# Optimization experiments

Hardware: AMD Instinct MI355X
Metric: run time of the kernel (lower is better)

Reference implementation:

```python
import jax, jax.numpy as jnp
import numpy as np
from jax import lax

L = 2048      # sentence length
V = 50000     # vocab size
E = 512       # embedding dim
HD = 512      # per-direction hidden (hidden_dim // 2)
H = 1024      # hidden_dim
T = 48        # tagset size
START, STOP = 46, 47
NEG = -10000.0


def setup_inputs() -> dict:
    key = jax.random.key(0)
    ks = iter(jax.random.split(key, 40))
    def n(shape, s=0.1):
        return jax.random.normal(next(ks), shape, dtype=jnp.float32) * s
    inp = {"sentence": jax.random.randint(next(ks), (L,), 0, V, dtype=jnp.int32)}
    inp["embedding"] = n((V, E), 1.0)
    for l, din in ((0, E), (1, H)):
        for d in ("", "r"):
            inp[f"w_ih_l{l}{d}"] = n((4 * HD, din))
            inp[f"w_hh_l{l}{d}"] = n((4 * HD, HD))
            inp[f"b_ih_l{l}{d}"] = n((4 * HD,))
            inp[f"b_hh_l{l}{d}"] = n((4 * HD,))
    inp["h0"] = n((4, HD), 1.0)
    inp["c0"] = n((4, HD), 1.0)
    inp["W_tag"] = n((T, H))
    inp["b_tag"] = n((T,))
    tr = n((T, T), 1.0)
    inp["transitions"] = tr.at[START, :].set(NEG).at[:, STOP].set(NEG)
    return inp


def _lstm_dir(x, w_ih, w_hh, b_ih, b_hh, h, c, reverse):
    # PyTorch LSTM cell, gates ordered (i, f, g, o). x: [L, Din]
    pre = x @ w_ih.T + (b_ih + b_hh)  # [L, 4*HD]
    def step(carry, p):
        h, c = carry
        g = p + h @ w_hh.T
        i, f, gg, o = jnp.split(g, 4)
        i, f, o = jax.nn.sigmoid(i), jax.nn.sigmoid(f), jax.nn.sigmoid(o)
        c = f * c + i * jnp.tanh(gg)
        h = o * jnp.tanh(c)
        return (h, c), h
    _, hs = lax.scan(step, (h, c), pre, reverse=reverse)
    return hs  # [L, HD], time-aligned with input


def _viterbi(feats, transitions):
    # max-plus recurrence over the tagset, vectorized per timestep
    init = jnp.full((T,), NEG, dtype=feats.dtype).at[START].set(0.0)
    def step(fv, feat):
        scores = fv[None, :] + transitions  # [next_tag, prev_tag]
        bp = jnp.argmax(scores, axis=1)
        return jnp.max(scores, axis=1) + feat, bp
    fv, bps = lax.scan(step, init, feats)  # bps: [L, T]
    terminal = fv + transitions[STOP]
    best = jnp.argmax(terminal)
    score = terminal[best]
    def back(tag, bp):
        prev = bp[tag]
        return prev, prev
    _, ys = lax.scan(back, best, bps, reverse=True)
    # ys[0] == START (dropped); path is tags for t = 0..L-1
    path = jnp.concatenate([ys[1:], best[None]])
    return score, path


def reference(sentence, embedding,
              w_ih_l0, w_hh_l0, b_ih_l0, b_hh_l0,
              w_ih_l0r, w_hh_l0r, b_ih_l0r, b_hh_l0r,
              w_ih_l1, w_hh_l1, b_ih_l1, b_hh_l1,
              w_ih_l1r, w_hh_l1r, b_ih_l1r, b_hh_l1r,
              h0, c0, W_tag, b_tag, transitions):
    embeds = embedding[sentence]  # [L, E]
    l0 = jnp.concatenate([
        _lstm_dir(embeds, w_ih_l0, w_hh_l0, b_ih_l0, b_hh_l0, h0[0], c0[0], False),
        _lstm_dir(embeds, w_ih_l0r, w_hh_l0r, b_ih_l0r, b_hh_l0r, h0[1], c0[1], True),
    ], axis=-1)  # [L, H]
    l1 = jnp.concatenate([
        _lstm_dir(l0, w_ih_l1, w_hh_l1, b_ih_l1, b_hh_l1, h0[2], c0[2], False),
        _lstm_dir(l0, w_ih_l1r, w_hh_l1r, b_ih_l1r, b_hh_l1r, h0[3], c0[3], True),
    ], axis=-1)  # [L, H]
    feats = l1 @ W_tag.T + b_tag  # [L, T]
    score, path = _viterbi(feats, transitions)
    return score, path
```

## Files before the change

kernel.cpp:

```cpp
#include <hip/hip_runtime.h>
#include <hip/hip_bf16.h>

#define L_SEQ 2048
#define HDIM 512
#define NGATE4 2048
#define TAGS 48
#define START_TAG 46
#define STOP_TAG 47
#define NWG 16

#define BM 64
#define BN 64
#define BK 32
#define LDT 68

__global__ __launch_bounds__(256, 2)
void gemm_abt(const float* __restrict__ A, const float* __restrict__ B,
              const float* __restrict__ bias1, const float* __restrict__ bias2,
              float* __restrict__ C, int M, int N, int K,
              const int* __restrict__ gather)
{
  __shared__ float As[BK][LDT];
  __shared__ float Bs[BK][LDT];
  const int tid = threadIdx.x;
  const int m0 = blockIdx.x * BM;
  const int n0 = blockIdx.y * BN;
  const int tm = tid >> 4, tn = tid & 15;
  const int lr = tid >> 2, lk = (tid & 3) * 8;

  float acc[4][4];
#pragma unroll
  for (int i = 0; i < 4; ++i)
#pragma unroll
    for (int c = 0; c < 4; ++c) acc[i][c] = 0.f;

  const int am = m0 + lr;
  const float* arow = gather ? (A + (size_t)gather[am] * (size_t)K)
                             : (A + (size_t)am * (size_t)K);
  const int bn = n0 + lr;
  const float* brow = B + (size_t)bn * (size_t)K;
  const bool bok = (bn < N);

  for (int kt = 0; kt < K; kt += BK) {
    const float4 a0 = *(const float4*)(arow + kt + lk);
    const float4 a1 = *(const float4*)(arow + kt + lk + 4);
    float4 b0 = make_float4(0.f, 0.f, 0.f, 0.f);
    float4 b1 = make_float4(0.f, 0.f, 0.f, 0.f);
    if (bok) {
      b0 = *(const float4*)(brow + kt + lk);
      b1 = *(const float4*)(brow + kt + lk + 4);
    }
    As[lk + 0][lr] = a0.x; As[lk + 1][lr] = a0.y; As[lk + 2][lr] = a0.z; As[lk + 3][lr] = a0.w;
    As[lk + 4][lr] = a1.x; As[lk + 5][lr] = a1.y; As[lk + 6][lr] = a1.z; As[lk + 7][lr] = a1.w;
    Bs[lk + 0][lr] = b0.x; Bs[lk + 1][lr] = b0.y; Bs[lk + 2][lr] = b0.z; Bs[lk + 3][lr] = b0.w;
    Bs[lk + 4][lr] = b1.x; Bs[lk + 5][lr] = b1.y; Bs[lk + 6][lr] = b1.z; Bs[lk + 7][lr] = b1.w;
    __syncthreads();
#pragma unroll
    for (int kk = 0; kk < BK; ++kk) {
      const float4 av = *(const float4*)&As[kk][tm * 4];
      const float4 bv = *(const float4*)&Bs[kk][tn * 4];
      const float aa[4] = {av.x, av.y, av.z, av.w};
      const float bb[4] = {bv.x, bv.y, bv.z, bv.w};
#pragma unroll
      for (int i = 0; i < 4; ++i)
#pragma unroll
        for (int c = 0; c < 4; ++c)
          acc[i][c] += aa[i] * bb[c];
    }
    __syncthreads();
  }

  float bsum[4];
#pragma unroll
  for (int c = 0; c < 4; ++c) {
    const int n = n0 + tn * 4 + c;
    float bb = 0.f;
    if (n < N) { bb = bias1[n]; if (bias2) bb += bias2[n]; }
    bsum[c] = bb;
  }
#pragma unroll
  for (int i = 0; i < 4; ++i) {
    const int m = m0 + tm * 4 + i;
#pragma unroll
    for (int c = 0; c < 4; ++c) {
      const int n = n0 + tn * 4 + c;
      if (n < N) C[(size_t)m * N + n] = acc[i][c] + bsum[c];
    }
  }
}

__global__ __launch_bounds__(512, 1)
void lstm_layer(const float* __restrict__ pre_f, const float* __restrict__ pre_r,
                const float* __restrict__ whh_f, const float* __restrict__ whh_r,
                const float* __restrict__ h0, const float* __restrict__ c0,
                int hcrow_base,
                float* __restrict__ hs_out,
                int* __restrict__ slots)
{
  const int dir = blockIdx.x & 1;
  const int wg  = blockIdx.x >> 1;
  const float* pre = dir ? pre_r : pre_f;
  const float* whh = dir ? whh_r : whh_f;
  int* myslots = slots + dir * NWG;
  const int tid = threadIdx.x;
  const int lane = tid & 63;
  const int wave = tid >> 6;
  const int q = lane & 15;
  const int jj = (wave << 2) | (lane >> 4);
  const int j = wg * 32 + jj;
  const bool leader = (q == 0);
  const int hc = (hcrow_base + dir) * HDIM;

  __shared__ float h_lds[HDIM];

  float w[4][8][4];
#pragma unroll
  for (int g = 0; g < 4; ++g) {
    const float* wr = whh + (size_t)(g * HDIM + j) * HDIM;
#pragma unroll
    for (int i = 0; i < 8; ++i) {
      const int kb = 32 * q + 4 * ((i + q) & 7);
      const float4 v = *(const float4*)(wr + kb);
      w[g][i][0] = v.x; w[g][i][1] = v.y; w[g][i][2] = v.z; w[g][i][3] = v.w;
    }
  }
  h_lds[tid] = h0[hc + tid];
  float cst = leader ? c0[hc + j] : 0.f;
  __syncthreads();

  float p[4], pn[4];
  {
    const int t0 = dir ? (L_SEQ - 1) : 0;
#pragma unroll
    for (int g = 0; g < 4; ++g)
      p[g] = leader ? pre[(size_t)t0 * NGATE4 + g * HDIM + j] : 0.f;
  }

  for (int s = 0; s < L_SEQ; ++s) {
    const int t = dir ? (L_SEQ - 1 - s) : s;
#pragma unroll
    for (int g = 0; g < 4; ++g) pn[g] = 0.f;
    if (leader && (s + 1 < L_SEQ)) {
      const int tnx = dir ? (L_SEQ - 2 - s) : (s + 1);
#pragma unroll
      for (int g = 0; g < 4; ++g)
        pn[g] = pre[(size_t)tnx * NGATE4 + g * HDIM + j];
    }

    float a[4] = {0.f, 0.f, 0.f, 0.f};
#pragma unroll
    for (int i = 0; i < 8; ++i) {
      const int kb = 32 * q + 4 * ((i + q) & 7);
      const float4 hv = *(const float4*)&h_lds[kb];
      const float hh[4] = {hv.x, hv.y, hv.z, hv.w};
#pragma unroll
      for (int g = 0; g < 4; ++g)
#pragma unroll
        for (int c = 0; c < 4; ++c)
          a[g] += w[g][i][c] * hh[c];
    }
#pragma unroll
    for (int m = 1; m < 16; m <<= 1)
#pragma unroll
      for (int g = 0; g < 4; ++g)
        a[g] += __shfl_xor(a[g], m, 64);

    if (leader) {
      const float gi = p[0] + a[0];
      const float gf = p[1] + a[1];
      const float gg = p[2] + a[2];
      const float go = p[3] + a[3];
      const float si = 1.f / (1.f + __expf(-gi));
      const float sf = 1.f / (1.f + __expf(-gf));
      const float tg = 1.f - 2.f / (__expf(2.f * gg) + 1.f);
      const float so = 1.f / (1.f + __expf(-go));
      cst = sf * cst + si * tg;
      const float th = 1.f - 2.f / (__expf(2.f * cst) + 1.f);
      const float h = so * th;
      __hip_atomic_store(&hs_out[(size_t)t * 1024 + dir * HDIM + j], h,
                         __ATOMIC_RELAXED, __HIP_MEMORY_SCOPE_AGENT);
    }
#pragma unroll
    for (int g = 0; g < 4; ++g) p[g] = pn[g];

    if (s == L_SEQ - 1) break;

    __syncthreads();
    if (tid == 0)
      __hip_atomic_store(&myslots[wg], s + 1, __ATOMIC_RELEASE,
                         __HIP_MEMORY_SCOPE_AGENT);
    if (wave == 0) {
      for (;;) {
        const int v = (lane < NWG)
            ? __hip_atomic_load(&myslots[lane], __ATOMIC_ACQUIRE,
                                __HIP_MEMORY_SCOPE_AGENT)
            : 0x7fffffff;
        if (__all(v > s)) break;
      }
    }
    __syncthreads();
    {
      const size_t base = (size_t)t * 1024 + dir * HDIM;
      h_lds[tid] = __hip_atomic_load(&hs_out[base + tid], __ATOMIC_RELAXED,
                                     __HIP_MEMORY_SCOPE_AGENT);
    }
    __syncthreads();
  }
}

__global__ __launch_bounds__(192, 1)
void viterbi_kernel(const float* __restrict__ feats,
                    const float* __restrict__ trans,
                    int* __restrict__ bp,
                    float* __restrict__ out)
{
  __shared__ float fv[TAGS];
  __shared__ float fvn[TAGS];
  const int tid = threadIdx.x;
  const int lane = tid & 63;
  const int wave = tid >> 6;
  const int q = lane & 3;
  const int j = wave * 16 + (lane >> 2);

  float trr[12];
#pragma unroll
  for (int kk = 0; kk < 12; ++kk) trr[kk] = trans[j * TAGS + q * 12 + kk];

  if (tid < TAGS) fv[tid] = (tid == START_TAG) ? 0.f : -10000.f;
  __syncthreads();

  for (int t = 0; t < L_SEQ; ++t) {
    const float ft = feats[t * TAGS + j];
    float best = -3.0e38f;
    int bi = 0;
#pragma unroll
    for (int kk = 0; kk < 12; ++kk) {
      const int k = q * 12 + kk;
      const float sc = fv[k] + trr[kk];
      if (sc > best) { best = sc; bi = k; }
    }
#pragma unroll
    for (int m = 1; m < 4; m <<= 1) {
      const float ov = __shfl_xor(best, m, 64);
      const int oi = __shfl_xor(bi, m, 64);
      if (ov > best || (ov == best && oi < bi)) { best = ov; bi = oi; }
    }
    __syncthreads();
    if (q == 0) {
      bp[t * TAGS + j] = bi;
      fv[j] = best + ft;
    }
    __syncthreads();
  }

  if (tid < TAGS) fvn[tid] = fv[tid] + trans[STOP_TAG * TAGS + tid];
  __syncthreads();
  if (tid == 0) {
    float best = -3.0e38f;
    int bi = 0;
    for (int k = 0; k < TAGS; ++k) {
      const float v = fvn[k];
      if (v > best) { best = v; bi = k; }
    }
    out[0] = best;
    int cur = bi;
    out[1 + (L_SEQ - 1)] = (float)cur;
    for (int t = L_SEQ - 2; t >= 0; --t) {
      cur = bp[(t + 1) * TAGS + cur];
      out[1 + t] = (float)cur;
    }
  }
}

extern "C" void kernel_launch(void* const* d_in, const int* in_sizes, int n_in,
                              void* d_out, int out_size, void* d_ws, size_t ws_size,
                              hipStream_t stream)
{
  const int*   sentence  = (const int*)  d_in[0];
  const float* embedding = (const float*)d_in[1];
  const float* w_ih_l0   = (const float*)d_in[2];
  const float* w_hh_l0   = (const float*)d_in[3];
  const float* b_ih_l0   = (const float*)d_in[4];
  const float* b_hh_l0   = (const float*)d_in[5];
  const float* w_ih_l0r  = (const float*)d_in[6];
  const float* w_hh_l0r  = (const float*)d_in[7];
  const float* b_ih_l0r  = (const float*)d_in[8];
  const float* b_hh_l0r  = (const float*)d_in[9];
  const float* w_ih_l1   = (const float*)d_in[10];
  const float* w_hh_l1   = (const float*)d_in[11];
  const float* b_ih_l1   = (const float*)d_in[12];
  const float* b_hh_l1   = (const float*)d_in[13];
  const float* w_ih_l1r  = (const float*)d_in[14];
  const float* w_hh_l1r  = (const float*)d_in[15];
  const float* b_ih_l1r  = (const float*)d_in[16];
  const float* b_hh_l1r  = (const float*)d_in[17];
  const float* h0        = (const float*)d_in[18];
  const float* c0        = (const float*)d_in[19];
  const float* W_tag     = (const float*)d_in[20];
  const float* b_tag     = (const float*)d_in[21];
  const float* trans     = (const float*)d_in[22];

  float* ws    = (float*)d_ws;
  float* pre_f = ws;
  float* pre_r = pre_f + (size_t)L_SEQ * NGATE4;
  float* l0out = pre_r + (size_t)L_SEQ * NGATE4;
  float* l1out = l0out + (size_t)L_SEQ * 1024;
  float* feats = l1out + (size_t)L_SEQ * 1024;
  int*   slots = (int*)(feats + (size_t)L_SEQ * TAGS);
  int*   bp    = slots + 4 * NWG;

  (void)hipMemsetAsync(slots, 0, 4 * NWG * sizeof(int), stream);

  dim3 blk(256);
  dim3 gfull(L_SEQ / BM, NGATE4 / BN);
  gemm_abt<<<gfull, blk, 0, stream>>>(embedding, w_ih_l0, b_ih_l0, b_hh_l0,
                                      pre_f, L_SEQ, NGATE4, 512, sentence);
  gemm_abt<<<gfull, blk, 0, stream>>>(embedding, w_ih_l0r, b_ih_l0r, b_hh_l0r,
                                      pre_r, L_SEQ, NGATE4, 512, sentence);
  lstm_layer<<<2 * NWG, 512, 0, stream>>>(pre_f, pre_r, w_hh_l0, w_hh_l0r,
                                          h0, c0, 0, l0out, slots);
  gemm_abt<<<gfull, blk, 0, stream>>>(l0out, w_ih_l1, b_ih_l1, b_hh_l1,
                                      pre_f, L_SEQ, NGATE4, 1024, nullptr);
  gemm_abt<<<gfull, blk, 0, stream>>>(l0out, w_ih_l1r, b_ih_l1r, b_hh_l1r,
                                      pre_r, L_SEQ, NGATE4, 1024, nullptr);
  lstm_layer<<<2 * NWG, 512, 0, stream>>>(pre_f, pre_r, w_hh_l1, w_hh_l1r,
                                          h0, c0, 2, l1out, slots + 2 * NWG);
  dim3 gfeat(L_SEQ / BM, 1);
  gemm_abt<<<gfeat, blk, 0, stream>>>(l1out, W_tag, b_tag, nullptr,
                                      feats, L_SEQ, TAGS, 1024, nullptr);
  viterbi_kernel<<<1, 192, 0, stream>>>(feats, trans, bp, (float*)d_out);
}
```

Before: 16.04 ms.

## Spread LSTM workgroups across XCDs and vectorize recurrent matvec accumulators

The recurrent LSTM kernel now launches 128 workgroups and keeps only those with blockIdx%8 in {0,1}. Round-robin dispatch should then place all 32 active workgroups on the same one or two XCDs, so the per-step cross-workgroup flag sync and h exchange stay within a shared L2 rather than crossing dies. The weight registers and matvec accumulation are also rewritten as float4 variables with per-lane float4 accumulators, reduced at the end, to aid register allocation and packed FMA. The extra idle workgroups add launch overhead, and the XCD placement depends on dispatch order, which the hardware does not guarantee.

```diff
diff --git a/kernel.cpp b/kernel.cpp
--- a/kernel.cpp
+++ b/kernel.cpp
@@ -8,6 +8,8 @@
 #define START_TAG 46
 #define STOP_TAG 47
 #define NWG 16
+
+typedef float4 f4;
 
 #define BM 64
 #define BN 64
@@ -89,6 +91,22 @@
   }
 }
 
+#define LOADW(g) { const float* wr = whh + (size_t)((g) * HDIM + j) * HDIM + 32 * q; \
+  w##g##0 = *(const f4*)(wr + 4 * ((0 + q) & 7)); \
+  w##g##1 = *(const f4*)(wr + 4 * ((1 + q) & 7)); \
+  w##g##2 = *(const f4*)(wr + 4 * ((2 + q) & 7)); \
+  w##g##3 = *(const f4*)(wr + 4 * ((3 + q) & 7)); \
+  w##g##4 = *(const f4*)(wr + 4 * ((4 + q) & 7)); \
+  w##g##5 = *(const f4*)(wr + 4 * ((5 + q) & 7)); \
+  w##g##6 = *(const f4*)(wr + 4 * ((6 + q) & 7)); \
+  w##g##7 = *(const f4*)(wr + 4 * ((7 + q) & 7)); }
+
+#define FMA4(A_, W_, H_) { A_.x += (W_).x * (H_).x; A_.y += (W_).y * (H_).y; \
+                           A_.z += (W_).z * (H_).z; A_.w += (W_).w * (H_).w; }
+
+#define FI(i) { const f4 hv_ = *(const f4*)&h_lds[32 * q + 4 * (((i) + q) & 7)]; \
+  FMA4(acc0, w0##i, hv_) FMA4(acc1, w1##i, hv_) FMA4(acc2, w2##i, hv_) FMA4(acc3, w3##i, hv_) }
+
 __global__ __launch_bounds__(512, 1)
 void lstm_layer(const float* __restrict__ pre_f, const float* __restrict__ pre_r,
                 const float* __restrict__ whh_f, const float* __restrict__ whh_r,
@@ -97,8 +115,10 @@
                 float* __restrict__ hs_out,
                 int* __restrict__ slots)
 {
-  const int dir = blockIdx.x & 1;
-  const int wg  = blockIdx.x >> 1;
+  const int sel = blockIdx.x & 7;
+  if (sel > 1) return;
+  const int dir = sel;
+  const int wg  = blockIdx.x >> 3;
   const float* pre = dir ? pre_r : pre_f;
   const float* whh = dir ? whh_r : whh_f;
   int* myslots = slots + dir * NWG;
@@ -113,63 +133,58 @@
 
   __shared__ float h_lds[HDIM];
 
-  float w[4][8][4];
-#pragma unroll
-  for (int g = 0; g < 4; ++g) {
-    const float* wr = whh + (size_t)(g * HDIM + j) * HDIM;
-#pragma unroll
-    for (int i = 0; i < 8; ++i) {
-      const int kb = 32 * q + 4 * ((i + q) & 7);
-      const float4 v = *(const float4*)(wr + kb);
-      w[g][i][0] = v.x; w[g][i][1] = v.y; w[g][i][2] = v.z; w[g][i][3] = v.w;
-    }
-  }
+  f4 w00, w01, w02, w03, w04, w05, w06, w07;
+  f4 w10, w11, w12, w13, w14, w15, w16, w17;
+  f4 w20, w21, w22, w23, w24, w25, w26, w27;
+  f4 w30, w31, w32, w33, w34, w35, w36, w37;
+  LOADW(0) LOADW(1) LOADW(2) LOADW(3)
+
   h_lds[tid] = h0[hc + tid];
   float cst = leader ? c0[hc + j] : 0.f;
   __syncthreads();
 
-  float p[4], pn[4];
+  float p0, p1, p2, p3;
   {
     const int t0 = dir ? (L_SEQ - 1) : 0;
-#pragma unroll
-    for (int g = 0; g < 4; ++g)
-      p[g] = leader ? pre[(size_t)t0 * NGATE4 + g * HDIM + j] : 0.f;
+    const float* pr = pre + (size_t)t0 * NGATE4 + j;
+    p0 = leader ? pr[0 * HDIM] : 0.f;
+    p1 = leader ? pr[1 * HDIM] : 0.f;
+    p2 = leader ? pr[2 * HDIM] : 0.f;
+    p3 = leader ? pr[3 * HDIM] : 0.f;
   }
 
   for (int s = 0; s < L_SEQ; ++s) {
     const int t = dir ? (L_SEQ - 1 - s) : s;
-#pragma unroll
-    for (int g = 0; g < 4; ++g) pn[g] = 0.f;
+    float pn0 = 0.f, pn1 = 0.f, pn2 = 0.f, pn3 = 0.f;
     if (leader && (s + 1 < L_SEQ)) {
       const int tnx = dir ? (L_SEQ - 2 - s) : (s + 1);
-#pragma unroll
-      for (int g = 0; g < 4; ++g)
-        pn[g] = pre[(size_t)tnx * NGATE4 + g * HDIM + j];
-    }
-
-    float a[4] = {0.f, 0.f, 0.f, 0.f};
-#pragma unroll
-    for (int i = 0; i < 8; ++i) {
-      const int kb = 32 * q + 4 * ((i + q) & 7);
-      const float4 hv = *(const float4*)&h_lds[kb];
-      const float hh[4] = {hv.x, hv.y, hv.z, hv.w};
-#pragma unroll
-      for (int g = 0; g < 4; ++g)
-#pragma unroll
-        for (int c = 0; c < 4; ++c)
-          a[g] += w[g][i][c] * hh[c];
-    }
-#pragma unroll
-    for (int m = 1; m < 16; m <<= 1)
-#pragma unroll
-      for (int g = 0; g < 4; ++g)
-        a[g] += __shfl_xor(a[g], m, 64);
+      const float* pr = pre + (size_t)tnx * NGATE4 + j;
+      pn0 = pr[0 * HDIM]; pn1 = pr[1 * HDIM];
+      pn2 = pr[2 * HDIM]; pn3 = pr[3 * HDIM];
+    }
+
+    f4 acc0 = make_float4(0.f, 0.f, 0.f, 0.f);
+    f4 acc1 = make_float4(0.f, 0.f, 0.f, 0.f);
+    f4 acc2 = make_float4(0.f, 0.f, 0.f, 0.f);
+    f4 acc3 = make_float4(0.f, 0.f, 0.f, 0.f);
+    FI(0) FI(1) FI(2) FI(3) FI(4) FI(5) FI(6) FI(7)
+    float a0 = acc0.x + acc0.y + acc0.z + acc0.w;
+    float a1 = acc1.x + acc1.y + acc1.z + acc1.w;
+    float a2 = acc2.x + acc2.y + acc2.z + acc2.w;
+    float a3 = acc3.x + acc3.y + acc3.z + acc3.w;
+#pragma unroll
+    for (int m = 1; m < 16; m <<= 1) {
+      a0 += __shfl_xor(a0, m, 64);
+      a1 += __shfl_xor(a1, m, 64);
+      a2 += __shfl_xor(a2, m, 64);
+      a3 += __shfl_xor(a3, m, 64);
+    }
 
     if (leader) {
-      const float gi = p[0] + a[0];
-      const float gf = p[1] + a[1];
-      const float gg = p[2] + a[2];
-      const float go = p[3] + a[3];
+      const float gi = p0 + a0;
+      const float gf = p1 + a1;
+      const float gg = p2 + a2;
+      const float go = p3 + a3;
       const float si = 1.f / (1.f + __expf(-gi));
       const float sf = 1.f / (1.f + __expf(-gf));
       const float tg = 1.f - 2.f / (__expf(2.f * gg) + 1.f);
@@ -180,8 +195,7 @@
       __hip_atomic_store(&hs_out[(size_t)t * 1024 + dir * HDIM + j], h,
                          __ATOMIC_RELAXED, __HIP_MEMORY_SCOPE_AGENT);
     }
-#pragma unroll
-    for (int g = 0; g < 4; ++g) p[g] = pn[g];
+    p0 = pn0; p1 = pn1; p2 = pn2; p3 = pn3;
 
     if (s == L_SEQ - 1) break;
 
@@ -317,14 +331,14 @@
                                       pre_f, L_SEQ, NGATE4, 512, sentence);
   gemm_abt<<<gfull, blk, 0, stream>>>(embedding, w_ih_l0r, b_ih_l0r, b_hh_l0r,
                                       pre_r, L_SEQ, NGATE4, 512, sentence);
-  lstm_layer<<<2 * NWG, 512, 0, stream>>>(pre_f, pre_r, w_hh_l0, w_hh_l0r,
-                                          h0, c0, 0, l0out, slots);
+  lstm_layer<<<128, 512, 0, stream>>>(pre_f, pre_r, w_hh_l0, w_hh_l0r,
+                                      h0, c0, 0, l0out, slots);
   gemm_abt<<<gfull, blk, 0, stream>>>(l0out, w_ih_l1, b_ih_l1, b_hh_l1,
                                       pre_f, L_SEQ, NGATE4, 1024, nullptr);
   gemm_abt<<<gfull, blk, 0, stream>>>(l0out, w_ih_l1r, b_ih_l1r, b_hh_l1r,
                                       pre_r, L_SEQ, NGATE4, 1024, nullptr);
-  lstm_layer<<<2 * NWG, 512, 0, stream>>>(pre_f, pre_r, w_hh_l1, w_hh_l1r,
-                                          h0, c0, 2, l1out, slots + 2 * NWG);
+  lstm_layer<<<128, 512, 0, stream>>>(pre_f, pre_r, w_hh_l1, w_hh_l1r,
+                                      h0, c0, 2, l1out, slots + 2 * NWG);
   dim3 gfeat(L_SEQ / BM, 1);
   gemm_abt<<<gfeat, blk, 0, stream>>>(l1out, W_tag, b_tag, nullptr,
                                       feats, L_SEQ, TAGS, 1024, nullptr);
```

Measured after the change: 18.10 ms. 1.13x slower.

## Spread LSTM recurrence over 64 workgroups per direction with LDS-resident weights

Applied to the files above, without the earlier changes.

Raises the number of workgroups per direction in the persistent LSTM recurrence from 16 to 64. Each wave now owns one hidden unit, with 16-lane groups per gate, and keeps its W_hh slice in shared memory instead of registers. Gates are combined through cross-lane shuffles. The goal is to cut per-step matvec latency by using more CUs and fewer registers per thread. In exchange, the grid-wide barrier has to poll four times as many slot flags each step, and weights are now read from LDS on every step.

```diff
diff --git a/kernel.cpp b/kernel.cpp
--- a/kernel.cpp
+++ b/kernel.cpp
@@ -7,7 +7,9 @@
 #define TAGS 48
 #define START_TAG 46
 #define STOP_TAG 47
-#define NWG 16
+#define NWG 64
+
+typedef float f32x4 __attribute__((ext_vector_type(4)));
 
 #define BM 64
 #define BN 64
@@ -106,82 +108,64 @@
   const int lane = tid & 63;
   const int wave = tid >> 6;
   const int q = lane & 15;
-  const int jj = (wave << 2) | (lane >> 4);
-  const int j = wg * 32 + jj;
-  const bool leader = (q == 0);
+  const int g = lane >> 4;
+  const int j = wg * 8 + wave;
   const int hc = (hcrow_base + dir) * HDIM;
 
+  __shared__ f32x4 wlds[8][8][64];
   __shared__ float h_lds[HDIM];
 
-  float w[4][8][4];
-#pragma unroll
-  for (int g = 0; g < 4; ++g) {
-    const float* wr = whh + (size_t)(g * HDIM + j) * HDIM;
-#pragma unroll
-    for (int i = 0; i < 8; ++i) {
-      const int kb = 32 * q + 4 * ((i + q) & 7);
-      const float4 v = *(const float4*)(wr + kb);
-      w[g][i][0] = v.x; w[g][i][1] = v.y; w[g][i][2] = v.z; w[g][i][3] = v.w;
-    }
+  {
+    const float* wr = whh + (size_t)(g * HDIM + j) * HDIM + 32 * q;
+#pragma unroll
+    for (int i = 0; i < 8; ++i)
+      wlds[wave][i][lane] = *(const f32x4*)(wr + 4 * ((i + q) & 7));
   }
   h_lds[tid] = h0[hc + tid];
-  float cst = leader ? c0[hc + j] : 0.f;
+  float cst = (lane == 0) ? c0[hc + j] : 0.f;
   __syncthreads();
 
-  float p[4], pn[4];
-  {
+  float p = 0.f;
+  if (q == 0) {
     const int t0 = dir ? (L_SEQ - 1) : 0;
-#pragma unroll
-    for (int g = 0; g < 4; ++g)
-      p[g] = leader ? pre[(size_t)t0 * NGATE4 + g * HDIM + j] : 0.f;
+    p = pre[(size_t)t0 * NGATE4 + g * HDIM + j];
   }
 
   for (int s = 0; s < L_SEQ; ++s) {
     const int t = dir ? (L_SEQ - 1 - s) : s;
-#pragma unroll
-    for (int g = 0; g < 4; ++g) pn[g] = 0.f;
-    if (leader && (s + 1 < L_SEQ)) {
+    float pn = 0.f;
+    if (q == 0 && (s + 1 < L_SEQ)) {
       const int tnx = dir ? (L_SEQ - 2 - s) : (s + 1);
-#pragma unroll
-      for (int g = 0; g < 4; ++g)
-        pn[g] = pre[(size_t)tnx * NGATE4 + g * HDIM + j];
-    }
-
-    float a[4] = {0.f, 0.f, 0.f, 0.f};
+      pn = pre[(size_t)tnx * NGATE4 + g * HDIM + j];
+    }
+
+    f32x4 acc = {0.f, 0.f, 0.f, 0.f};
 #pragma unroll
     for (int i = 0; i < 8; ++i) {
-      const int kb = 32 * q + 4 * ((i + q) & 7);
-      const float4 hv = *(const float4*)&h_lds[kb];
-      const float hh[4] = {hv.x, hv.y, hv.z, hv.w};
-#pragma unroll
-      for (int g = 0; g < 4; ++g)
-#pragma unroll
-        for (int c = 0; c < 4; ++c)
-          a[g] += w[g][i][c] * hh[c];
-    }
-#pragma unroll
-    for (int m = 1; m < 16; m <<= 1)
-#pragma unroll
-      for (int g = 0; g < 4; ++g)
-        a[g] += __shfl_xor(a[g], m, 64);
-
-    if (leader) {
-      const float gi = p[0] + a[0];
-      const float gf = p[1] + a[1];
-      const float gg = p[2] + a[2];
-      const float go = p[3] + a[3];
-      const float si = 1.f / (1.f + __expf(-gi));
-      const float sf = 1.f / (1.f + __expf(-gf));
-      const float tg = 1.f - 2.f / (__expf(2.f * gg) + 1.f);
-      const float so = 1.f / (1.f + __expf(-go));
+      const f32x4 wv = wlds[wave][i][lane];
+      const f32x4 hv = *(const f32x4*)&h_lds[32 * q + 4 * ((i + q) & 7)];
+      acc += wv * hv;
+    }
+    float a = acc.x + acc.y + acc.z + acc.w;
+#pragma unroll
+    for (int m = 1; m < 16; m <<= 1) a += __shfl_xor(a, m, 64);
+    a += p;
+
+    const float a1 = __shfl(a, 16, 64);
+    const float a2 = __shfl(a, 32, 64);
+    const float a3 = __shfl(a, 48, 64);
+    if (lane == 0) {
+      const float si = 1.f / (1.f + __expf(-a));
+      const float sf = 1.f / (1.f + __expf(-a1));
+      const float tg = 1.f - 2.f / (__expf(2.f * a2) + 1.f);
+      const float so = 1.f / (1.f + __expf(-a3));
       cst = sf * cst + si * tg;
       const float th = 1.f - 2.f / (__expf(2.f * cst) + 1.f);
       const float h = so * th;
       __hip_atomic_store(&hs_out[(size_t)t * 1024 + dir * HDIM + j], h,
                          __ATOMIC_RELAXED, __HIP_MEMORY_SCOPE_AGENT);
     }
-#pragma unroll
-    for (int g = 0; g < 4; ++g) p[g] = pn[g];
+    p = pn;
 
     if (s == L_SEQ - 1) break;
 
@@ -191,10 +175,8 @@
                          __HIP_MEMORY_SCOPE_AGENT);
     if (wave == 0) {
       for (;;) {
-        const int v = (lane < NWG)
-            ? __hip_atomic_load(&myslots[lane], __ATOMIC_ACQUIRE,
-                                __HIP_MEMORY_SCOPE_AGENT)
-            : 0x7fffffff;
+        const int v = __hip_atomic_load(&myslots[lane], __ATOMIC_ACQUIRE,
+                                        __HIP_MEMORY_SCOPE_AGENT);
         if (__all(v > s)) break;
       }
     }
```

New measurement: 24.52 ms. 52.8% more time.
